# Kernel tuning notes

Measured on AMD Instinct MI355X. Metric: run time of the kernel, lower is better.

The kernel has to match this reference:

```python
import jax, jax.numpy as jnp
import numpy as np

N_NODES = 100000
N_EDGES = 1200000
D_NODE = 64
D_EDGE = 64
HIDDEN = 128
EPS = 1e-5


def setup_inputs() -> dict:
    key = jax.random.key(0)
    ks = jax.random.split(key, 10)
    d_in = D_NODE + D_EDGE  # 128
    s0 = 1.0 / np.sqrt(d_in)
    s1 = 1.0 / np.sqrt(HIDDEN)
    return {
        "x": jax.random.normal(ks[0], (N_NODES, D_NODE), dtype=jnp.float32),
        "edge_index": jax.random.randint(ks[1], (2, N_EDGES), 0, N_NODES, dtype=jnp.int64),
        "edge_attr": jax.random.normal(ks[2], (N_EDGES, D_EDGE), dtype=jnp.float32),
        # MLP params: Linear(d_in,H) -> ReLU -> Linear(H,H) -> ReLU -> Linear(H,D_NODE) -> LayerNorm
        "W0": jax.random.uniform(ks[3], (d_in, HIDDEN), jnp.float32, -s0, s0),
        "b0": jnp.zeros((HIDDEN,), jnp.float32),
        "W1": jax.random.uniform(ks[4], (HIDDEN, HIDDEN), jnp.float32, -s1, s1),
        "b1": jnp.zeros((HIDDEN,), jnp.float32),
        "W2": jax.random.uniform(ks[5], (HIDDEN, D_NODE), jnp.float32, -s1, s1),
        "b2": jnp.zeros((D_NODE,), jnp.float32),
        "ln_g": jnp.ones((D_NODE,), jnp.float32),
        "ln_b": jnp.zeros((D_NODE,), jnp.float32),
    }


def _layer_norm(h, g, b):
    mu = jnp.mean(h, axis=-1, keepdims=True)
    var = jnp.mean(jnp.square(h - mu), axis=-1, keepdims=True)
    return (h - mu) * jax.lax.rsqrt(var + EPS) * g + b


def reference(x, edge_index, edge_attr, W0, b0, W1, b1, W2, b2, ln_g, ln_b):
    col = edge_index[1]
    # scatter_sum(edge_attr, col, dim=0): segment sum over destination nodes -> [N, D_EDGE]
    agg = jax.ops.segment_sum(edge_attr, col, num_segments=N_NODES)
    h = jnp.concatenate([x, agg], axis=-1)  # [N, D_NODE + D_EDGE]
    h = jax.nn.relu(h @ W0 + b0)
    h = jax.nn.relu(h @ W1 + b1)
    h = h @ W2 + b2
    h = _layer_norm(h, ln_g, ln_b)
    return h + x
```

## Files before the change

### kernel.cpp

```cpp
#include <hip/hip_runtime.h>

#define NNODES 100000
#define DN 64
#define SROW 136

typedef short bf16x8 __attribute__((ext_vector_type(8)));
typedef float f32x4 __attribute__((ext_vector_type(4)));

__device__ __forceinline__ unsigned short f2bf(float f) {
  unsigned int u = __float_as_uint(f);
  u = (u + 0x7fffu + ((u >> 16) & 1u)) >> 16;
  return (unsigned short)u;
}
__device__ __forceinline__ float bf2f(unsigned short h) {
  return __uint_as_float(((unsigned int)h) << 16);
}

__global__ __launch_bounds__(256) void hist_kernel(const int* __restrict__ col,
                                                   int* __restrict__ deg, int n) {
  int i = blockIdx.x * 256 + threadIdx.x;
  if (i < n) atomicAdd(&deg[col[i]], 1);
}

__global__ __launch_bounds__(1024) void scan_blk(const int* __restrict__ deg,
                                                 int* __restrict__ bsum) {
  __shared__ int red[1024];
  int t = threadIdx.x;
  int i = blockIdx.x * 1024 + t;
  red[t] = (i < NNODES) ? deg[i] : 0;
  __syncthreads();
  for (int off = 512; off > 0; off >>= 1) {
    if (t < off) red[t] += red[t + off];
    __syncthreads();
  }
  if (t == 0) bsum[blockIdx.x] = red[0];
}

__global__ __launch_bounds__(128) void scan_top(int* __restrict__ bsum) {
  __shared__ int tmp[128];
  int t = threadIdx.x;
  if (t < 98) tmp[t] = bsum[t];
  __syncthreads();
  if (t == 0) {
    int run = 0;
    for (int i = 0; i < 98; ++i) { int v = tmp[i]; tmp[i] = run; run += v; }
  }
  __syncthreads();
  if (t < 98) bsum[t] = tmp[t];
}

__global__ __launch_bounds__(1024) void scan_fin(const int* __restrict__ deg,
                                                 const int* __restrict__ bsum,
                                                 int* __restrict__ row_ptr,
                                                 int* __restrict__ cursor) {
  __shared__ int ps[1024];
  int t = threadIdx.x;
  int i = blockIdx.x * 1024 + t;
  int v = (i < NNODES) ? deg[i] : 0;
  ps[t] = v;
  __syncthreads();
  for (int off = 1; off < 1024; off <<= 1) {
    int u = (t >= off) ? ps[t - off] : 0;
    __syncthreads();
    ps[t] += u;
    __syncthreads();
  }
  int excl = ps[t] - v + bsum[blockIdx.x];
  if (i < NNODES) { row_ptr[i] = excl; cursor[i] = excl; }
  if (i == NNODES - 1) row_ptr[NNODES] = excl + v;
}

__global__ __launch_bounds__(256) void fillconv_kernel(
    const int* __restrict__ col, const float* __restrict__ ea,
    int* __restrict__ cursor, unsigned short* __restrict__ sorted, int n) {
  int t = blockIdx.x * 256 + threadIdx.x;
  int e = t >> 4;
  if (e >= n) return;
  const int sub = t & 15;
  const int lane = threadIdx.x & 63;
  int d = col[e];
  int pos = 0;
  if (sub == 0) pos = atomicAdd(&cursor[d], 1);
  pos = __shfl(pos, lane & 48);
  float4 v = *(const float4*)(ea + (size_t)e * 64 + sub * 4);
  ushort4 o;
  o.x = f2bf(v.x); o.y = f2bf(v.y); o.z = f2bf(v.z); o.w = f2bf(v.w);
  *(ushort4*)(sorted + (size_t)pos * 64 + sub * 4) = o;
}

__global__ __launch_bounds__(256) void gather_kernel(
    const int* __restrict__ row_ptr, const unsigned short* __restrict__ sorted,
    unsigned short* __restrict__ aggb) {
  const int wid = threadIdx.x >> 6;
  const int lane = threadIdx.x & 63;
  const int node = blockIdx.x * 4 + wid;
  if (node >= NNODES) return;
  const int s = row_ptr[node], e = row_ptr[node + 1];
  const int ch0 = (lane & 7) * 8;
  float acc[8];
#pragma unroll
  for (int k = 0; k < 8; ++k) acc[k] = 0.f;
  for (int j = s + (lane >> 3); j < e; j += 8) {
    bf16x8 v = *(const bf16x8*)(sorted + (size_t)j * 64 + ch0);
#pragma unroll
    for (int k = 0; k < 8; ++k) acc[k] += bf2f((unsigned short)v[k]);
  }
#pragma unroll
  for (int msk = 8; msk < 64; msk <<= 1)
#pragma unroll
    for (int k = 0; k < 8; ++k) acc[k] += __shfl_xor(acc[k], msk);
  if (lane < 8) {
    bf16x8 o;
#pragma unroll
    for (int k = 0; k < 8; ++k) o[k] = (short)f2bf(acc[k]);
    *(bf16x8*)(aggb + (size_t)node * 64 + lane * 8) = o;
  }
}

__global__ __launch_bounds__(256) void wprep_kernel(
    const float* __restrict__ W0, const float* __restrict__ W1,
    const float* __restrict__ W2, unsigned short* __restrict__ wp) {
  int t = blockIdx.x * 256 + threadIdx.x;
  if (t >= 5120) return;
  const float* W; int c, N, dstbase;
  if (t < 2048)      { W = W0; c = t;        N = 128; dstbase = 0; }
  else if (t < 4096) { W = W1; c = t - 2048; N = 128; dstbase = 16384; }
  else               { W = W2; c = t - 4096; N = 64;  dstbase = 32768; }
  int blk = c >> 6;
  int lane = c & 63;
  int nc = blk >> 2, kc = blk & 3;
  int k0 = kc * 32 + (lane >> 4) * 8;
  int n  = nc * 16 + (lane & 15);
  unsigned short* dst = wp + dstbase + blk * 512 + lane * 8;
#pragma unroll
  for (int j = 0; j < 8; ++j) dst[j] = f2bf(W[(size_t)(k0 + j) * N + n]);
}

__global__ __launch_bounds__(256) void fused_mlp(
    const float* __restrict__ x, const unsigned short* __restrict__ aggb,
    const unsigned short* __restrict__ wp,
    const float* __restrict__ b0, const float* __restrict__ b1,
    const float* __restrict__ b2, const float* __restrict__ lng,
    const float* __restrict__ lnb, float* __restrict__ out) {
  __shared__ unsigned short act[4 * 2 * 16 * SROW];

  const int tid = threadIdx.x;
  const int wid = tid >> 6;
  const int lane = tid & 63;
  const int gw = blockIdx.x * 4 + wid;
  if (gw >= NNODES / 16) return;
  const int base = gw * 16;
  const int m = lane & 15;
  const int quad = lane >> 4;

  unsigned short* Abuf = act + (wid * 2 + 0) * 16 * SROW;
  unsigned short* Bbuf = act + (wid * 2 + 1) * 16 * SROW;

#pragma unroll 4
  for (int r = 0; r < 16; ++r) {
    int node = base + r;
    Abuf[r * SROW + lane] = f2bf(x[(size_t)node * 64 + lane]);
    Abuf[r * SROW + 64 + lane] = aggb[(size_t)node * 64 + lane];
  }

  bf16x8 af[4];

#pragma unroll
  for (int kc = 0; kc < 4; ++kc)
    af[kc] = *(const bf16x8*)(Abuf + m * SROW + kc * 32 + quad * 8);
#pragma unroll
  for (int nc = 0; nc < 8; ++nc) {
    float bv = b0[nc * 16 + m];
    f32x4 acc = {bv, bv, bv, bv};
#pragma unroll
    for (int kc = 0; kc < 4; ++kc) {
      bf16x8 bf = *(const bf16x8*)(wp + (nc * 4 + kc) * 512 + lane * 8);
      acc = __builtin_amdgcn_mfma_f32_16x16x32_bf16(af[kc], bf, acc, 0, 0, 0);
    }
    int col = nc * 16 + m;
#pragma unroll
    for (int r2 = 0; r2 < 4; ++r2)
      Bbuf[(quad * 4 + r2) * SROW + col] = f2bf(fmaxf(acc[r2], 0.f));
  }

#pragma unroll
  for (int kc = 0; kc < 4; ++kc)
    af[kc] = *(const bf16x8*)(Bbuf + m * SROW + kc * 32 + quad * 8);
#pragma unroll
  for (int nc = 0; nc < 8; ++nc) {
    float bv = b1[nc * 16 + m];
    f32x4 acc = {bv, bv, bv, bv};
#pragma unroll
    for (int kc = 0; kc < 4; ++kc) {
      bf16x8 bf = *(const bf16x8*)(wp + 16384 + (nc * 4 + kc) * 512 + lane * 8);
      acc = __builtin_amdgcn_mfma_f32_16x16x32_bf16(af[kc], bf, acc, 0, 0, 0);
    }
    int col = nc * 16 + m;
#pragma unroll
    for (int r2 = 0; r2 < 4; ++r2)
      Abuf[(quad * 4 + r2) * SROW + col] = f2bf(fmaxf(acc[r2], 0.f));
  }

#pragma unroll
  for (int kc = 0; kc < 4; ++kc)
    af[kc] = *(const bf16x8*)(Abuf + m * SROW + kc * 32 + quad * 8);
  f32x4 acc2[4];
#pragma unroll
  for (int nc = 0; nc < 4; ++nc) {
    float bv = b2[nc * 16 + m];
    f32x4 acc = {bv, bv, bv, bv};
#pragma unroll
    for (int kc = 0; kc < 4; ++kc) {
      bf16x8 bf = *(const bf16x8*)(wp + 32768 + (nc * 4 + kc) * 512 + lane * 8);
      acc = __builtin_amdgcn_mfma_f32_16x16x32_bf16(af[kc], bf, acc, 0, 0, 0);
    }
    acc2[nc] = acc;
  }

  float s[4], ss[4];
#pragma unroll
  for (int r2 = 0; r2 < 4; ++r2) {
    float a0 = acc2[0][r2], a1 = acc2[1][r2], a2 = acc2[2][r2], a3 = acc2[3][r2];
    s[r2]  = a0 + a1 + a2 + a3;
    ss[r2] = a0 * a0 + a1 * a1 + a2 * a2 + a3 * a3;
  }
#pragma unroll
  for (int msk = 1; msk < 16; msk <<= 1) {
#pragma unroll
    for (int r2 = 0; r2 < 4; ++r2) {
      s[r2]  += __shfl_xor(s[r2], msk);
      ss[r2] += __shfl_xor(ss[r2], msk);
    }
  }
  float mu[4], rs[4];
#pragma unroll
  for (int r2 = 0; r2 < 4; ++r2) {
    mu[r2] = s[r2] * 0.015625f;
    float var = ss[r2] * 0.015625f - mu[r2] * mu[r2];
    rs[r2] = rsqrtf(var + 1e-5f);
  }
#pragma unroll
  for (int nc = 0; nc < 4; ++nc) {
    int col = nc * 16 + m;
    float g = lng[col], bb = lnb[col];
#pragma unroll
    for (int r2 = 0; r2 < 4; ++r2) {
      int node = base + quad * 4 + r2;
      float xr = x[(size_t)node * 64 + col];
      out[(size_t)node * 64 + col] =
          (acc2[nc][r2] - mu[r2]) * rs[r2] * g + bb + xr;
    }
  }
}

extern "C" void kernel_launch(void* const* d_in, const int* in_sizes, int n_in,
                              void* d_out, int out_size, void* d_ws, size_t ws_size,
                              hipStream_t stream) {
  const float* x  = (const float*)d_in[0];
  const int*   ei = (const int*)d_in[1];
  const float* ea = (const float*)d_in[2];
  const float* W0 = (const float*)d_in[3];
  const float* b0 = (const float*)d_in[4];
  const float* W1 = (const float*)d_in[5];
  const float* b1 = (const float*)d_in[6];
  const float* W2 = (const float*)d_in[7];
  const float* b2 = (const float*)d_in[8];
  const float* lg = (const float*)d_in[9];
  const float* lb = (const float*)d_in[10];
  float* out = (float*)d_out;

  const int n_edges = in_sizes[2] / DN;
  const int* col = ei + n_edges;

  char* ws = (char*)d_ws;
  int* deg     = (int*)(ws + 0);
  int* row_ptr = (int*)(ws + 400000);
  int* cursor  = (int*)(ws + 800016);
  int* bsum    = (int*)(ws + 1200016);
  unsigned short* wp   = (unsigned short*)(ws + 1200512);
  unsigned short* aggb = (unsigned short*)(ws + 1282432);
  unsigned short* sorted = (unsigned short*)(ws + 14083072);

  hipMemsetAsync(deg, 0, NNODES * sizeof(int), stream);

  hist_kernel<<<(n_edges + 255) / 256, 256, 0, stream>>>(col, deg, n_edges);
  scan_blk<<<98, 1024, 0, stream>>>(deg, bsum);
  scan_top<<<1, 128, 0, stream>>>(bsum);
  scan_fin<<<98, 1024, 0, stream>>>(deg, bsum, row_ptr, cursor);
  wprep_kernel<<<20, 256, 0, stream>>>(W0, W1, W2, wp);

  fillconv_kernel<<<(n_edges * 16 + 255) / 256, 256, 0, stream>>>(
      col, ea, cursor, sorted, n_edges);

  gather_kernel<<<(NNODES + 3) / 4, 256, 0, stream>>>(row_ptr, sorted, aggb);

  int nblocks = (NNODES / 16 + 3) / 4;
  fused_mlp<<<nblocks, 256, 0, stream>>>(x, aggb, wp, b0, b1, b2, lg, lb, out);
}
```

Measured before the change: 584.9 us.

## Replace CSR sort-and-gather aggregation with direct fp32 atomic scatter-add

Drops the histogram, three-stage scan, counting-sort fill and per-node gather kernels. Each edge feature element is instead atomically added into a zeroed fp32 aggregate buffer, which the MLP kernel reads and converts to bf16. This removes several launches and the intermediate sorted bf16 copy. In exchange it issues 76.8M fp32 atomics to random destinations, and the summation order becomes nondeterministic.

```diff
diff --git a/kernel.cpp b/kernel.cpp
--- a/kernel.cpp
+++ b/kernel.cpp
@@ -16,105 +16,16 @@
   return __uint_as_float(((unsigned int)h) << 16);
 }
 
-__global__ __launch_bounds__(256) void hist_kernel(const int* __restrict__ col,
-                                                   int* __restrict__ deg, int n) {
-  int i = blockIdx.x * 256 + threadIdx.x;
-  if (i < n) atomicAdd(&deg[col[i]], 1);
-}
-
-__global__ __launch_bounds__(1024) void scan_blk(const int* __restrict__ deg,
-                                                 int* __restrict__ bsum) {
-  __shared__ int red[1024];
-  int t = threadIdx.x;
-  int i = blockIdx.x * 1024 + t;
-  red[t] = (i < NNODES) ? deg[i] : 0;
-  __syncthreads();
-  for (int off = 512; off > 0; off >>= 1) {
-    if (t < off) red[t] += red[t + off];
-    __syncthreads();
-  }
-  if (t == 0) bsum[blockIdx.x] = red[0];
-}
-
-__global__ __launch_bounds__(128) void scan_top(int* __restrict__ bsum) {
-  __shared__ int tmp[128];
-  int t = threadIdx.x;
-  if (t < 98) tmp[t] = bsum[t];
-  __syncthreads();
-  if (t == 0) {
-    int run = 0;
-    for (int i = 0; i < 98; ++i) { int v = tmp[i]; tmp[i] = run; run += v; }
-  }
-  __syncthreads();
-  if (t < 98) bsum[t] = tmp[t];
-}
-
-__global__ __launch_bounds__(1024) void scan_fin(const int* __restrict__ deg,
-                                                 const int* __restrict__ bsum,
-                                                 int* __restrict__ row_ptr,
-                                                 int* __restrict__ cursor) {
-  __shared__ int ps[1024];
-  int t = threadIdx.x;
-  int i = blockIdx.x * 1024 + t;
-  int v = (i < NNODES) ? deg[i] : 0;
-  ps[t] = v;
-  __syncthreads();
-  for (int off = 1; off < 1024; off <<= 1) {
-    int u = (t >= off) ? ps[t - off] : 0;
-    __syncthreads();
-    ps[t] += u;
-    __syncthreads();
-  }
-  int excl = ps[t] - v + bsum[blockIdx.x];
-  if (i < NNODES) { row_ptr[i] = excl; cursor[i] = excl; }
-  if (i == NNODES - 1) row_ptr[NNODES] = excl + v;
-}
-
-__global__ __launch_bounds__(256) void fillconv_kernel(
+__global__ __launch_bounds__(256) void scatter_kernel(
     const int* __restrict__ col, const float* __restrict__ ea,
-    int* __restrict__ cursor, unsigned short* __restrict__ sorted, int n) {
+    float* __restrict__ agg, int n) {
   int t = blockIdx.x * 256 + threadIdx.x;
-  int e = t >> 4;
+  int e = t >> 6;
   if (e >= n) return;
-  const int sub = t & 15;
-  const int lane = threadIdx.x & 63;
+  int c = t & 63;
   int d = col[e];
-  int pos = 0;
-  if (sub == 0) pos = atomicAdd(&cursor[d], 1);
-  pos = __shfl(pos, lane & 48);
-  float4 v = *(const float4*)(ea + (size_t)e * 64 + sub * 4);
-  ushort4 o;
-  o.x = f2bf(v.x); o.y = f2bf(v.y); o.z = f2bf(v.z); o.w = f2bf(v.w);
-  *(ushort4*)(sorted + (size_t)pos * 64 + sub * 4) = o;
-}
-
-__global__ __launch_bounds__(256) void gather_kernel(
-    const int* __restrict__ row_ptr, const unsigned short* __restrict__ sorted,
-    unsigned short* __restrict__ aggb) {
-  const int wid = threadIdx.x >> 6;
-  const int lane = threadIdx.x & 63;
-  const int node = blockIdx.x * 4 + wid;
-  if (node >= NNODES) return;
-  const int s = row_ptr[node], e = row_ptr[node + 1];
-  const int ch0 = (lane & 7) * 8;
-  float acc[8];
-#pragma unroll
-  for (int k = 0; k < 8; ++k) acc[k] = 0.f;
-  for (int j = s + (lane >> 3); j < e; j += 8) {
-    bf16x8 v = *(const bf16x8*)(sorted + (size_t)j * 64 + ch0);
-#pragma unroll
-    for (int k = 0; k < 8; ++k) acc[k] += bf2f((unsigned short)v[k]);
-  }
-#pragma unroll
-  for (int msk = 8; msk < 64; msk <<= 1)
-#pragma unroll
-    for (int k = 0; k < 8; ++k) acc[k] += __shfl_xor(acc[k], msk);
-  if (lane < 8) {
-    bf16x8 o;
-#pragma unroll
-    for (int k = 0; k < 8; ++k) o[k] = (short)f2bf(acc[k]);
-    *(bf16x8*)(aggb + (size_t)node * 64 + lane * 8) = o;
-  }
+  float v = ea[(size_t)e * 64 + c];
+  atomicAdd(agg + (size_t)d * 64 + c, v);
 }
 
 __global__ __launch_bounds__(256) void wprep_kernel(
@@ -137,7 +48,7 @@
 }
 
 __global__ __launch_bounds__(256) void fused_mlp(
-    const float* __restrict__ x, const unsigned short* __restrict__ aggb,
+    const float* __restrict__ x, const float* __restrict__ agg,
     const unsigned short* __restrict__ wp,
     const float* __restrict__ b0, const float* __restrict__ b1,
     const float* __restrict__ b2, const float* __restrict__ lng,
@@ -160,7 +71,7 @@
   for (int r = 0; r < 16; ++r) {
     int node = base + r;
     Abuf[r * SROW + lane] = f2bf(x[(size_t)node * 64 + lane]);
-    Abuf[r * SROW + 64 + lane] = aggb[(size_t)node * 64 + lane];
+    Abuf[r * SROW + 64 + lane] = f2bf(agg[(size_t)node * 64 + lane]);
   }
 
   bf16x8 af[4];
@@ -273,27 +184,16 @@
   const int* col = ei + n_edges;
 
   char* ws = (char*)d_ws;
-  int* deg     = (int*)(ws + 0);
-  int* row_ptr = (int*)(ws + 400000);
-  int* cursor  = (int*)(ws + 800016);
-  int* bsum    = (int*)(ws + 1200016);
-  unsigned short* wp   = (unsigned short*)(ws + 1200512);
-  unsigned short* aggb = (unsigned short*)(ws + 1282432);
-  unsigned short* sorted = (unsigned short*)(ws + 14083072);
+  unsigned short* wp = (unsigned short*)(ws + 0);
+  float* agg = (float*)(ws + 81920);
 
-  hipMemsetAsync(deg, 0, NNODES * sizeof(int), stream);
+  hipMemsetAsync(agg, 0, (size_t)NNODES * DN * sizeof(float), stream);
 
-  hist_kernel<<<(n_edges + 255) / 256, 256, 0, stream>>>(col, deg, n_edges);
-  scan_blk<<<98, 1024, 0, stream>>>(deg, bsum);
-  scan_top<<<1, 128, 0, stream>>>(bsum);
-  scan_fin<<<98, 1024, 0, stream>>>(deg, bsum, row_ptr, cursor);
   wprep_kernel<<<20, 256, 0, stream>>>(W0, W1, W2, wp);
 
-  fillconv_kernel<<<(n_edges * 16 + 255) / 256, 256, 0, stream>>>(
-      col, ea, cursor, sorted, n_edges);
-
-  gather_kernel<<<(NNODES + 3) / 4, 256, 0, stream>>>(row_ptr, sorted, aggb);
+  scatter_kernel<<<(n_edges * 64 + 255) / 256, 256, 0, stream>>>(
+      col, ea, agg, n_edges);
 
   int nblocks = (NNODES / 16 + 3) / 4;
-  fused_mlp<<<nblocks, 256, 0, stream>>>(x, aggb, wp, b0, b1, b2, lg, lb, out);
+  fused_mlp<<<nblocks, 256, 0, stream>>>(x, agg, wp, b0, b1, b2, lg, lb, out);
 }
```

Result: slower. 621.5 us (+6.3%).

## Sort edge indices instead of edge features and gather fp32 rows directly

Applied to the files above, without the earlier changes.

Replaces the pass that converted and scattered edge_attr into a bf16 sorted copy with a pass that only scatters edge ids into CSR order. The gather kernel then reads the fp32 edge_attr rows indirectly through those ids and writes fp32 aggregates, which the MLP converts to bf16 on load. This removes one full write and one full read of the edge-feature array, at the cost of an indirect, non-sequential row read and a wider fp32 aggregate buffer.

```diff
diff --git a/kernel.cpp b/kernel.cpp
--- a/kernel.cpp
+++ b/kernel.cpp
@@ -70,50 +70,42 @@
   if (i == NNODES - 1) row_ptr[NNODES] = excl + v;
 }
 
-__global__ __launch_bounds__(256) void fillconv_kernel(
-    const int* __restrict__ col, const float* __restrict__ ea,
-    int* __restrict__ cursor, unsigned short* __restrict__ sorted, int n) {
-  int t = blockIdx.x * 256 + threadIdx.x;
-  int e = t >> 4;
+__global__ __launch_bounds__(256) void fill_eid(
+    const int* __restrict__ col, int* __restrict__ cursor,
+    int* __restrict__ eid, int n) {
+  int e = blockIdx.x * 256 + threadIdx.x;
   if (e >= n) return;
-  const int sub = t & 15;
-  const int lane = threadIdx.x & 63;
   int d = col[e];
-  int pos = 0;
-  if (sub == 0) pos = atomicAdd(&cursor[d], 1);
-  pos = __shfl(pos, lane & 48);
-  float4 v = *(const float4*)(ea + (size_t)e * 64 + sub * 4);
-  ushort4 o;
-  o.x = f2bf(v.x); o.y = f2bf(v.y); o.z = f2bf(v.z); o.w = f2bf(v.w);
-  *(ushort4*)(sorted + (size_t)pos * 64 + sub * 4) = o;
+  int pos = atomicAdd(&cursor[d], 1);
+  eid[pos] = e;
 }
 
 __global__ __launch_bounds__(256) void gather_kernel(
-    const int* __restrict__ row_ptr, const unsigned short* __restrict__ sorted,
-    unsigned short* __restrict__ aggb) {
+    const int* __restrict__ row_ptr, const int* __restrict__ eid,
+    const float* __restrict__ ea, float* __restrict__ agg) {
   const int wid = threadIdx.x >> 6;
   const int lane = threadIdx.x & 63;
   const int node = blockIdx.x * 4 + wid;
   if (node >= NNODES) return;
   const int s = row_ptr[node], e = row_ptr[node + 1];
-  const int ch0 = (lane & 7) * 8;
-  float acc[8];
-#pragma unroll
-  for (int k = 0; k < 8; ++k) acc[k] = 0.f;
-  for (int j = s + (lane >> 3); j < e; j += 8) {
-    bf16x8 v = *(const bf16x8*)(sorted + (size_t)j * 64 + ch0);
-#pragma unroll
-    for (int k = 0; k < 8; ++k) acc[k] += bf2f((unsigned short)v[k]);
-  }
-#pragma unroll
-  for (int msk = 8; msk < 64; msk <<= 1)
-#pragma unroll
-    for (int k = 0; k < 8; ++k) acc[k] += __shfl_xor(acc[k], msk);
-  if (lane < 8) {
-    bf16x8 o;
-#pragma unroll
-    for (int k = 0; k < 8; ++k) o[k] = (short)f2bf(acc[k]);
-    *(bf16x8*)(aggb + (size_t)node * 64 + lane * 8) = o;
+  const int slot = lane >> 4;
+  const int c4 = (lane & 15) * 4;
+  float a0 = 0.f, a1 = 0.f, a2 = 0.f, a3 = 0.f;
+  for (int j = s + slot; j < e; j += 4) {
+    int ev = eid[j];
+    float4 v = *(const float4*)(ea + (size_t)ev * 64 + c4);
+    a0 += v.x; a1 += v.y; a2 += v.z; a3 += v.w;
+  }
+#pragma unroll
+  for (int msk = 16; msk < 64; msk <<= 1) {
+    a0 += __shfl_xor(a0, msk);
+    a1 += __shfl_xor(a1, msk);
+    a2 += __shfl_xor(a2, msk);
+    a3 += __shfl_xor(a3, msk);
+  }
+  if (lane < 16) {
+    float4 o = {a0, a1, a2, a3};
+    *(float4*)(agg + (size_t)node * 64 + c4) = o;
   }
 }
 
@@ -137,7 +129,7 @@
 }
 
 __global__ __launch_bounds__(256) void fused_mlp(
-    const float* __restrict__ x, const unsigned short* __restrict__ aggb,
+    const float* __restrict__ x, const float* __restrict__ agg,
     const unsigned short* __restrict__ wp,
     const float* __restrict__ b0, const float* __restrict__ b1,
     const float* __restrict__ b2, const float* __restrict__ lng,
@@ -160,7 +152,7 @@
   for (int r = 0; r < 16; ++r) {
     int node = base + r;
     Abuf[r * SROW + lane] = f2bf(x[(size_t)node * 64 + lane]);
-    Abuf[r * SROW + 64 + lane] = aggb[(size_t)node * 64 + lane];
+    Abuf[r * SROW + 64 + lane] = f2bf(agg[(size_t)node * 64 + lane]);
   }
 
   bf16x8 af[4];
@@ -277,9 +269,9 @@
   int* row_ptr = (int*)(ws + 400000);
   int* cursor  = (int*)(ws + 800016);
   int* bsum    = (int*)(ws + 1200016);
-  unsigned short* wp   = (unsigned short*)(ws + 1200512);
-  unsigned short* aggb = (unsigned short*)(ws + 1282432);
-  unsigned short* sorted = (unsigned short*)(ws + 14083072);
+  unsigned short* wp = (unsigned short*)(ws + 1200512);
+  int* eid     = (int*)(ws + 1282432);
+  float* agg   = (float*)(ws + 6082432);
 
   hipMemsetAsync(deg, 0, NNODES * sizeof(int), stream);
 
@@ -289,11 +281,10 @@
   scan_fin<<<98, 1024, 0, stream>>>(deg, bsum, row_ptr, cursor);
   wprep_kernel<<<20, 256, 0, stream>>>(W0, W1, W2, wp);
 
-  fillconv_kernel<<<(n_edges * 16 + 255) / 256, 256, 0, stream>>>(
-      col, ea, cursor, sorted, n_edges);
-
-  gather_kernel<<<(NNODES + 3) / 4, 256, 0, stream>>>(row_ptr, sorted, aggb);
+  fill_eid<<<(n_edges + 255) / 256, 256, 0, stream>>>(col, cursor, eid, n_edges);
+
+  gather_kernel<<<(NNODES + 3) / 4, 256, 0, stream>>>(row_ptr, eid, ea, agg);
 
   int nblocks = (NNODES / 16 + 3) / 4;
-  fused_mlp<<<nblocks, 256, 0, stream>>>(x, aggb, wp, b0, b1, b2, lg, lb, out);
-}
+  fused_mlp<<<nblocks, 256, 0, stream>>>(x, agg, wp, b0, b1, b2, lg, lb, out);
+}
```

New measurement: 646.8 us. +10.6%, slower.

## Fuse segment-sum gather into MLP kernel and widen fill-convert per-thread vectors

Applied to the files above, without the earlier changes.

Removes the separate gather kernel and its aggb intermediate. The fused MLP now reads row_ptr and sums each node's sorted bf16 edge rows directly into shared memory, one lane per channel, looping over edges serially per row. The fill-convert kernel now handles 8 channels per thread with nontemporal loads and stores, halving its thread count. The trade-off is that the in-MLP gather gets less parallelism per node (sequential edges across 16 rows per wave) in exchange for one fewer launch and one fewer round-trip through global memory.

```diff
diff --git a/kernel.cpp b/kernel.cpp
--- a/kernel.cpp
+++ b/kernel.cpp
@@ -5,6 +5,7 @@
 #define SROW 136
 
 typedef short bf16x8 __attribute__((ext_vector_type(8)));
+typedef unsigned short u16x8 __attribute__((ext_vector_type(8)));
 typedef float f32x4 __attribute__((ext_vector_type(4)));
 
 __device__ __forceinline__ unsigned short f2bf(float f) {
@@ -74,47 +75,20 @@
     const int* __restrict__ col, const float* __restrict__ ea,
     int* __restrict__ cursor, unsigned short* __restrict__ sorted, int n) {
   int t = blockIdx.x * 256 + threadIdx.x;
-  int e = t >> 4;
+  int e = t >> 3;
   if (e >= n) return;
-  const int sub = t & 15;
+  const int sub = t & 7;
   const int lane = threadIdx.x & 63;
-  int d = col[e];
   int pos = 0;
-  if (sub == 0) pos = atomicAdd(&cursor[d], 1);
-  pos = __shfl(pos, lane & 48);
-  float4 v = *(const float4*)(ea + (size_t)e * 64 + sub * 4);
-  ushort4 o;
-  o.x = f2bf(v.x); o.y = f2bf(v.y); o.z = f2bf(v.z); o.w = f2bf(v.w);
-  *(ushort4*)(sorted + (size_t)pos * 64 + sub * 4) = o;
-}
-
-__global__ __launch_bounds__(256) void gather_kernel(
-    const int* __restrict__ row_ptr, const unsigned short* __restrict__ sorted,
-    unsigned short* __restrict__ aggb) {
-  const int wid = threadIdx.x >> 6;
-  const int lane = threadIdx.x & 63;
-  const int node = blockIdx.x * 4 + wid;
-  if (node >= NNODES) return;
-  const int s = row_ptr[node], e = row_ptr[node + 1];
-  const int ch0 = (lane & 7) * 8;
-  float acc[8];
-#pragma unroll
-  for (int k = 0; k < 8; ++k) acc[k] = 0.f;
-  for (int j = s + (lane >> 3); j < e; j += 8) {
-    bf16x8 v = *(const bf16x8*)(sorted + (size_t)j * 64 + ch0);
-#pragma unroll
-    for (int k = 0; k < 8; ++k) acc[k] += bf2f((unsigned short)v[k]);
-  }
-#pragma unroll
-  for (int msk = 8; msk < 64; msk <<= 1)
-#pragma unroll
-    for (int k = 0; k < 8; ++k) acc[k] += __shfl_xor(acc[k], msk);
-  if (lane < 8) {
-    bf16x8 o;
-#pragma unroll
-    for (int k = 0; k < 8; ++k) o[k] = (short)f2bf(acc[k]);
-    *(bf16x8*)(aggb + (size_t)node * 64 + lane * 8) = o;
-  }
+  if (sub == 0) pos = atomicAdd(&cursor[col[e]], 1);
+  pos = __shfl(pos, lane & 56);
+  const f32x4* src = (const f32x4*)(ea + (size_t)e * 64 + sub * 8);
+  f32x4 v0 = __builtin_nontemporal_load(src);
+  f32x4 v1 = __builtin_nontemporal_load(src + 1);
+  u16x8 o;
+  o[0] = f2bf(v0[0]); o[1] = f2bf(v0[1]); o[2] = f2bf(v0[2]); o[3] = f2bf(v0[3]);
+  o[4] = f2bf(v1[0]); o[5] = f2bf(v1[1]); o[6] = f2bf(v1[2]); o[7] = f2bf(v1[3]);
+  __builtin_nontemporal_store(o, (u16x8*)(sorted + (size_t)pos * 64 + sub * 8));
 }
 
 __global__ __launch_bounds__(256) void wprep_kernel(
@@ -137,7 +111,8 @@
 }
 
 __global__ __launch_bounds__(256) void fused_mlp(
-    const float* __restrict__ x, const unsigned short* __restrict__ aggb,
+    const float* __restrict__ x, const int* __restrict__ row_ptr,
+    const unsigned short* __restrict__ sorted,
     const unsigned short* __restrict__ wp,
     const float* __restrict__ b0, const float* __restrict__ b1,
     const float* __restrict__ b2, const float* __restrict__ lng,
@@ -156,11 +131,19 @@
   unsigned short* Abuf = act + (wid * 2 + 0) * 16 * SROW;
   unsigned short* Bbuf = act + (wid * 2 + 1) * 16 * SROW;
 
+  int rp = 0;
+  if (lane < 17) rp = row_ptr[base + lane];
+
 #pragma unroll 4
+  for (int r = 0; r < 16; ++r)
+    Abuf[r * SROW + lane] = f2bf(x[(size_t)(base + r) * 64 + lane]);
+
   for (int r = 0; r < 16; ++r) {
-    int node = base + r;
-    Abuf[r * SROW + lane] = f2bf(x[(size_t)node * 64 + lane]);
-    Abuf[r * SROW + 64 + lane] = aggb[(size_t)node * 64 + lane];
+    int s = __shfl(rp, r), e = __shfl(rp, r + 1);
+    float acc = 0.f;
+    for (int j = s; j < e; ++j)
+      acc += bf2f(sorted[(size_t)j * 64 + lane]);
+    Abuf[r * SROW + 64 + lane] = f2bf(acc);
   }
 
   bf16x8 af[4];
@@ -277,11 +260,10 @@
   int* row_ptr = (int*)(ws + 400000);
   int* cursor  = (int*)(ws + 800016);
   int* bsum    = (int*)(ws + 1200016);
-  unsigned short* wp   = (unsigned short*)(ws + 1200512);
-  unsigned short* aggb = (unsigned short*)(ws + 1282432);
-  unsigned short* sorted = (unsigned short*)(ws + 14083072);
-
-  hipMemsetAsync(deg, 0, NNODES * sizeof(int), stream);
+  unsigned short* wp = (unsigned short*)(ws + 1200512);
+  unsigned short* sorted = (unsigned short*)(ws + 1282432);
+
+  (void)hipMemsetAsync(deg, 0, NNODES * sizeof(int), stream);
 
   hist_kernel<<<(n_edges + 255) / 256, 256, 0, stream>>>(col, deg, n_edges);
   scan_blk<<<98, 1024, 0, stream>>>(deg, bsum);
@@ -289,11 +271,10 @@
   scan_fin<<<98, 1024, 0, stream>>>(deg, bsum, row_ptr, cursor);
   wprep_kernel<<<20, 256, 0, stream>>>(W0, W1, W2, wp);
 
-  fillconv_kernel<<<(n_edges * 16 + 255) / 256, 256, 0, stream>>>(
+  fillconv_kernel<<<(n_edges * 8 + 255) / 256, 256, 0, stream>>>(
       col, ea, cursor, sorted, n_edges);
 
-  gather_kernel<<<(NNODES + 3) / 4, 256, 0, stream>>>(row_ptr, sorted, aggb);
-
   int nblocks = (NNODES / 16 + 3) / 4;
-  fused_mlp<<<nblocks, 256, 0, stream>>>(x, aggb, wp, b0, b1, b2, lg, lb, out);
-}
+  fused_mlp<<<nblocks, 256, 0, stream>>>(x, row_ptr, sorted, wp,
+                                         b0, b1, b2, lg, lb, out);
+}
```

After: 726.2 us. 1.24x slower.
